# Optimization experiments

Hardware: AMD Instinct MI355X
Metric: run time of the kernel (lower is better)

Reference implementation:

```python
import jax, jax.numpy as jnp
import numpy as np

B, C, R, E, H = 32, 64, 63, 256, 4
D = E // H  # head dim = 64


def setup_inputs() -> dict:
    key = jax.random.key(0)
    ks = jax.random.split(key, 8)
    s = 0.02
    return {
        "x": jax.random.normal(ks[0], (B, C, R, E), jnp.float32),
        "real_cols": jax.random.randint(ks[1], (B,), 0, C),
        "cls_token": jax.random.normal(ks[2], (E,), jnp.float32),
        "w_in": (jax.random.normal(ks[3], (3 * E, E), jnp.float32) * s),
        "b_in": jnp.zeros((3 * E,), jnp.float32),
        "w_out": (jax.random.normal(ks[4], (E, E), jnp.float32) * s),
        "b_out": jnp.zeros((E,), jnp.float32),
        "ln_g": jnp.ones((E,), jnp.float32),
        "ln_b": jnp.zeros((E,), jnp.float32),
        "w1": (jax.random.normal(ks[5], (E, E), jnp.float32) * s),
        "b1": jnp.zeros((E,), jnp.float32),
        "w2": (jax.random.normal(ks[6], (E, E), jnp.float32) * s),
        "b2": jnp.zeros((E,), jnp.float32),
    }


def reference(x, real_cols, cls_token, w_in, b_in, w_out, b_out, ln_g, ln_b, w1, b1, w2, b2):
    # x: (B, C, R, E); one fused batched MHA+LN+FFN over all (B, C) columns.
    Bq, Cq, Rq, Eq = x.shape
    S = Rq + 1
    cls = jnp.broadcast_to(cls_token, (Bq, Cq, 1, Eq))
    seq = jnp.concatenate([cls, x], axis=2)  # (B,C,S,E)

    # torch MultiheadAttention in-projection: x @ W^T + b, packed q|k|v
    qkv = seq @ w_in.T + b_in  # (B,C,S,3E)
    q, k, v = jnp.split(qkv, 3, axis=-1)
    q = q.reshape(Bq, Cq, S, H, D)
    k = k.reshape(Bq, Cq, S, H, D)
    v = v.reshape(Bq, Cq, S, H, D)

    scale = 1.0 / jnp.sqrt(jnp.asarray(D, x.dtype))
    scores = jnp.einsum('bcqhd,bckhd->bchqk', q, k) * scale  # (B,C,H,S,S)
    attn = jax.nn.softmax(scores, axis=-1)
    ctx = jnp.einsum('bchqk,bckhd->bcqhd', attn, v).reshape(Bq, Cq, S, Eq)
    attn_out = ctx @ w_out.T + b_out  # (B,C,S,E)

    # LayerNorm (biased variance, eps=1e-5 as in torch)
    mu = attn_out.mean(axis=-1, keepdims=True)
    var = ((attn_out - mu) ** 2).mean(axis=-1, keepdims=True)
    ln = (attn_out - mu) / jnp.sqrt(var + 1e-5) * ln_g + ln_b

    ffn = jax.nn.relu(ln @ w1.T + b1) @ w2.T + b2
    out = ln + ffn  # (B,C,S,E)

    rep = out[:, :, 0, :]  # rep_mode == 'cls'

    # columns >= real_cols[b] are zero-padded, matching the original loop
    mask = jnp.arange(Cq)[None, :] < real_cols[:, None]
    return jnp.where(mask[..., None], rep, jnp.zeros((), x.dtype))
```

## Files before the change

### kernel.cpp

```cpp
#include <hip/hip_runtime.h>
#include <hip/hip_bf16.h>
#include <cstdint>

typedef unsigned short u16;
typedef uint32_t u32;

#define Bq 32
#define Cq 64
#define Rq 63
#define NB 4
#define SEQ_ST 264

typedef __attribute__((ext_vector_type(8))) short bf16x8;
typedef __attribute__((ext_vector_type(4))) float f32x4;

__device__ __forceinline__ float bflo(u32 u){ return __uint_as_float(u << 16); }
__device__ __forceinline__ float bfhi(u32 u){ return __uint_as_float(u & 0xffff0000u); }
__device__ __forceinline__ float bf1(u16 u){ return __uint_as_float(((u32)u) << 16); }
__device__ __forceinline__ u16 tobf(float f){ __hip_bfloat16 h = __float2bfloat16(f); return *(u16*)&h; }

__device__ __forceinline__ bool dtype_is_bf16(const void* ln_g){
    return *(const u32*)ln_g == 0x3F803F80u;
}
__device__ __forceinline__ float ldin(const void* p, int i, bool bf){
    return bf ? bf1(((const u16*)p)[i]) : ((const float*)p)[i];
}


__global__ __launch_bounds__(256) void prep_kernel(
    const void* __restrict__ cls, const void* __restrict__ w_in,
    const void* __restrict__ b_in, const void* __restrict__ w_out,
    const void* __restrict__ w1, const void* __restrict__ w2,
    const void* __restrict__ ln_g_flag,
    float* __restrict__ uf, float* __restrict__ sbf,
    u16* __restrict__ wvT, u16* __restrict__ woT,
    u16* __restrict__ w1T, u16* __restrict__ w2T)
{
    const bool bf = dtype_is_bf16(ln_g_flag);
    const int tid = threadIdx.x;
    const int blk = blockIdx.x;
    __shared__ float q0[256];
    __shared__ __align__(16) float clsf[256];

    if (blk < 256) {
        const int e = blk, j = tid;
        const int dsti = (((e >> 4) * 512) + ((j >> 5) * 64) + (((j >> 3) & 3) * 16) + (e & 15)) * 8 + (j & 7);
        wvT[dsti] = tobf(ldin(w_in, (512 + e) * 256 + j, bf));
        woT[dsti] = tobf(ldin(w_out, e * 256 + j, bf));
        w1T[dsti] = tobf(ldin(w1,    e * 256 + j, bf));
        w2T[dsti] = tobf(ldin(w2,    e * 256 + j, bf));
        return;
    }

    const int h = blk - 256;
    clsf[tid] = ldin(cls, tid, bf);
    __syncthreads();

    {
        float acc = ldin(b_in, tid, bf);
        if (bf) {
            const u16* wr = (const u16*)w_in + tid * 256;
            #pragma unroll 8
            for (int j8 = 0; j8 < 32; ++j8) {
                uint4 w = *(const uint4*)(wr + j8 * 8);
                const float* c = &clsf[j8 * 8];
                acc += bflo(w.x) * c[0] + bfhi(w.x) * c[1]
                     + bflo(w.y) * c[2] + bfhi(w.y) * c[3]
                     + bflo(w.z) * c[4] + bfhi(w.z) * c[5]
                     + bflo(w.w) * c[6] + bfhi(w.w) * c[7];
            }
        } else {
            const float4* wr = (const float4*)((const float*)w_in + tid * 256);
            #pragma unroll 8
            for (int j4 = 0; j4 < 64; ++j4) {
                float4 w = wr[j4];
                float4 c = *(const float4*)&clsf[j4 * 4];
                acc += w.x * c.x + w.y * c.y + w.z * c.z + w.w * c.w;
            }
        }
        q0[tid] = acc;
    }
    __syncthreads();

    {
        float ua = 0.f;
        #pragma unroll 8
        for (int d = 0; d < 64; ++d)
            ua += q0[h * 64 + d] * ldin(w_in, (256 + h * 64 + d) * 256 + tid, bf);
        uf[h * 256 + tid] = ua * 0.125f;
    }
    if (tid < 64) {
        float p = q0[h * 64 + tid] * ldin(b_in, 256 + h * 64 + tid, bf);
        #pragma unroll
        for (int off = 32; off; off >>= 1) p += __shfl_xor(p, off);
        if (tid == 0) sbf[h] = p * 0.125f;
    }
}

__device__ __forceinline__ void mfma_layer4(const u16* __restrict__ wbase,
                                            const u16* __restrict__ Abase,
                                            int lane, int w,
                                            f32x4 acc[4])
{
    bf16x8 af[8];
    const u16* ap = Abase + (lane & 15) * SEQ_ST + (lane >> 4) * 8;
    #pragma unroll
    for (int ks = 0; ks < 8; ++ks)
        af[ks] = *(const bf16x8*)(ap + ks * 32);
    const u16* wp0 = wbase + (((w * 4) * 512 + lane) << 3);
    #pragma unroll
    for (int ks = 0; ks < 8; ++ks) {
        #pragma unroll
        for (int nt = 0; nt < 4; ++nt) {
            bf16x8 bfr = *(const bf16x8*)(wp0 + ((nt * 512 + ks * 64) << 3));
            acc[nt] = __builtin_amdgcn_mfma_f32_16x16x32_bf16(af[ks], bfr, acc[nt], 0, 0, 0);
        }
    }
}

__global__ __launch_bounds__(256) void fused_kernel(
    const void* __restrict__ x, const int* __restrict__ real_cols,
    const void* __restrict__ cls,
    const void* __restrict__ b_in, const void* __restrict__ b_out,
    const void* __restrict__ ln_g, const void* __restrict__ ln_b,
    const void* __restrict__ b1p, const void* __restrict__ b2p,
    const float* __restrict__ uf, const float* __restrict__ sbf,
    const u16* __restrict__ wvT, const u16* __restrict__ woT,
    const u16* __restrict__ w1T, const u16* __restrict__ w2T,
    void* __restrict__ out)
{
    const bool bf = dtype_is_bf16(ln_g);
    const int tid = threadIdx.x;
    const int b = blockIdx.x >> 4;
    const int g = blockIdx.x & 15;
    const int c0 = g * NB;
    const int rc = real_cols[b];
    const int e = tid;

    if (c0 >= rc) {
        #pragma unroll
        for (int i = 0; i < NB; ++i) {
            size_t oi = (((size_t)b << 6) + c0 + i) * 256 + e;
            if (bf) ((u16*)out)[oi] = 0; else ((float*)out)[oi] = 0.f;
        }
        return;
    }

    __shared__ __align__(16) char smem[53840];
    u16*   seq    = (u16*)smem;
    u16*   ctxB   = (u16*)smem;
    float* aoF    = (float*)(smem + 8448);
    u16*   lnB    = (u16*)(smem + 12544);
    u16*   h1B    = (u16*)(smem + 20992);
    float* lds_u  = (float*)(smem + 33792);
    float* lds_a  = (float*)(smem + 37888);
    float* lds_sb = (float*)(smem + 38912);
    u16*   sB     = (u16*)(smem + 38928);
    float* redA   = (float*)(smem + 53712);
    float* redB   = (float*)(smem + 53776);

    #pragma unroll
    for (int q = 0; q < 4; ++q) lds_u[q * 256 + tid] = uf[q * 256 + tid];
    if (tid < 4) lds_sb[tid] = sbf[tid];

    if (bf) {
        if (tid < 32) {
            uint4 val = *(const uint4*)((const u16*)cls + tid * 8);
            *(uint4*)&seq[tid * 8] = val;
        }
    } else {
        if (tid < 64) {
            float4 v = *(const float4*)((const float*)cls + tid * 4);
            u32 lo = ((u32)tobf(v.y) << 16) | tobf(v.x);
            u32 hi = ((u32)tobf(v.w) << 16) | tobf(v.z);
            *(uint2*)&seq[tid * 4] = make_uint2(lo, hi);
        }
    }

    const int w = tid >> 6, lane = tid & 63;

    uint4 stg[8];
    float4 stgf[16];
    auto load_col = [&](int c) {
        int bc2 = (b << 6) + c;
        if (bf) {
            const u16* xr = (const u16*)x + (size_t)bc2 * (Rq * 256);
            #pragma unroll
            for (int k = 0; k < 8; ++k) {
                int idx = k * 256 + tid;
                if (idx < 2016) stg[k] = *(const uint4*)(xr + idx * 8);
            }
        } else {
            const float* xr = (const float*)x + (size_t)bc2 * (Rq * 256);
            #pragma unroll
            for (int k = 0; k < 16; ++k) {
                int idx = k * 256 + tid;
                if (idx < 4032) stgf[k] = *(const float4*)(xr + idx * 4);
            }
        }
    };
    auto write_col = [&]() {
        if (bf) {
            #pragma unroll
            for (int k = 0; k < 8; ++k) {
                int idx = k * 256 + tid;
                if (idx < 2016) {
                    int tt = (idx >> 5) + 1, col = (idx & 31) * 8;
                    *(uint4*)&seq[tt * SEQ_ST + col] = stg[k];
                }
            }
        } else {
            #pragma unroll
            for (int k = 0; k < 16; ++k) {
                int idx = k * 256 + tid;
                if (idx < 4032) {
                    float4 v = stgf[k];
                    int tt = (idx >> 6) + 1, col = (idx & 63) * 4;
                    u32 lo = ((u32)tobf(v.y) << 16) | tobf(v.x);
                    u32 hi = ((u32)tobf(v.w) << 16) | tobf(v.z);
                    *(uint2*)&seq[tt * SEQ_ST + col] = make_uint2(lo, hi);
                }
            }
        }
    };

    load_col(c0);

    for (int i = 0; i < NB; ++i) {
        const int c = c0 + i;
        const bool act = (c < rc);

        if (act) write_col();
        __syncthreads();

        if (i + 1 < NB && c0 + i + 1 < rc) load_col(c0 + i + 1);

        if (act) {
            float sc = lds_sb[w];
            {
                const u16* srow = &seq[lane * SEQ_ST];
                const float* uh = &lds_u[w * 256];
                #pragma unroll 4
                for (int j = 0; j < 256; j += 8) {
                    uint4 pv = *(const uint4*)(srow + j);
                    float4 u0 = *(const float4*)(uh + j);
                    float4 u1 = *(const float4*)(uh + j + 4);
                    sc += bflo(pv.x) * u0.x + bfhi(pv.x) * u0.y
                        + bflo(pv.y) * u0.z + bfhi(pv.y) * u0.w
                        + bflo(pv.z) * u1.x + bfhi(pv.z) * u1.y
                        + bflo(pv.w) * u1.z + bfhi(pv.w) * u1.w;
                }
            }
            float m = sc;
            #pragma unroll
            for (int off = 32; off; off >>= 1) m = fmaxf(m, __shfl_xor(m, off));
            float ev = __expf(sc - m);
            float sum = ev;
            #pragma unroll
            for (int off = 32; off; off >>= 1) sum += __shfl_xor(sum, off);
            lds_a[lane * 4 + w] = ev / sum;
        }
        __syncthreads();

        if (act) {
            float s0 = 0.f, s1 = 0.f, s2 = 0.f, s3 = 0.f;
            #pragma unroll 4
            for (int tt = 0; tt < 64; ++tt) {
                float v = bf1(seq[tt * SEQ_ST + tid]);
                float4 at = *(const float4*)&lds_a[tt * 4];
                s0 += at.x * v; s1 += at.y * v; s2 += at.z * v; s3 += at.w * v;
            }
            sB[(0  + i) * SEQ_ST + tid] = tobf(s0);
            sB[(4  + i) * SEQ_ST + tid] = tobf(s1);
            sB[(8  + i) * SEQ_ST + tid] = tobf(s2);
            sB[(12 + i) * SEQ_ST + tid] = tobf(s3);
        } else {
            sB[(0  + i) * SEQ_ST + tid] = 0;
            sB[(4  + i) * SEQ_ST + tid] = 0;
            sB[(8  + i) * SEQ_ST + tid] = 0;
            sB[(12 + i) * SEQ_ST + tid] = 0;
        }
        __syncthreads();
    }

    f32x4 acc[4];

    #pragma unroll
    for (int nt = 0; nt < 4; ++nt) {
        float bv = ldin(b_in, 512 + w * 64 + nt * 16 + (lane & 15), bf);
        acc[nt] = (f32x4){bv, bv, bv, bv};
    }
    mfma_layer4(wvT, sB + w * 4 * SEQ_ST, lane, w, acc);
    if (lane < 16) {
        #pragma unroll
        for (int nt = 0; nt < 4; ++nt) {
            int n = w * 64 + nt * 16 + lane;
            #pragma unroll
            for (int r = 0; r < 4; ++r) ctxB[r * SEQ_ST + n] = tobf(acc[nt][r]);
        }
    }
    __syncthreads();

    #pragma unroll
    for (int nt = 0; nt < 4; ++nt) {
        float bv = ldin(b_out, w * 64 + nt * 16 + (lane & 15), bf);
        acc[nt] = (f32x4){bv, bv, bv, bv};
    }
    mfma_layer4(woT, ctxB, lane, w, acc);
    if (lane < 16) {
        #pragma unroll
        for (int nt = 0; nt < 4; ++nt) {
            int n = w * 64 + nt * 16 + lane;
            #pragma unroll
            for (int r = 0; r < 4; ++r) aoF[r * 256 + n] = acc[nt][r];
        }
    }
    __syncthreads();

    float ao[NB];
    #pragma unroll
    for (int i = 0; i < NB; ++i) ao[i] = aoF[i * 256 + e];

    float mu[NB];
    {
        float r[NB];
        #pragma unroll
        for (int i = 0; i < NB; ++i) r[i] = ao[i];
        #pragma unroll
        for (int off = 32; off; off >>= 1) {
            #pragma unroll
            for (int i = 0; i < NB; ++i) r[i] += __shfl_xor(r[i], off);
        }
        if (lane == 0) {
            #pragma unroll
            for (int i = 0; i < NB; ++i) redA[w * NB + i] = r[i];
        }
    }
    __syncthreads();
    #pragma unroll
    for (int i = 0; i < NB; ++i)
        mu[i] = (redA[i] + redA[NB + i] + redA[2 * NB + i] + redA[3 * NB + i]) * (1.f / 256.f);

    float lnv[NB];
    {
        float r[NB];
        #pragma unroll
        for (int i = 0; i < NB; ++i) { float d = ao[i] - mu[i]; r[i] = d * d; }
        #pragma unroll
        for (int off = 32; off; off >>= 1) {
            #pragma unroll
            for (int i = 0; i < NB; ++i) r[i] += __shfl_xor(r[i], off);
        }
        if (lane == 0) {
            #pragma unroll
            for (int i = 0; i < NB; ++i) redB[w * NB + i] = r[i];
        }
    }
    __syncthreads();
    {
        float gg = ldin(ln_g, e, bf), bb = ldin(ln_b, e, bf);
        #pragma unroll
        for (int i = 0; i < NB; ++i) {
            float var = (redB[i] + redB[NB + i] + redB[2 * NB + i] + redB[3 * NB + i]) * (1.f / 256.f);
            lnv[i] = (ao[i] - mu[i]) * rsqrtf(var + 1e-5f) * gg + bb;
            lnB[i * SEQ_ST + e] = tobf(lnv[i]);
        }
    }
    __syncthreads();

    #pragma unroll
    for (int nt = 0; nt < 4; ++nt) {
        float bv = ldin(b1p, w * 64 + nt * 16 + (lane & 15), bf);
        acc[nt] = (f32x4){bv, bv, bv, bv};
    }
    mfma_layer4(w1T, lnB, lane, w, acc);
    if (lane < 16) {
        #pragma unroll
        for (int nt = 0; nt < 4; ++nt) {
            int n = w * 64 + nt * 16 + lane;
            #pragma unroll
            for (int r = 0; r < 4; ++r) h1B[r * SEQ_ST + n] = tobf(fmaxf(acc[nt][r], 0.f));
        }
    }
    __syncthreads();

    #pragma unroll
    for (int nt = 0; nt < 4; ++nt) {
        float bv = ldin(b2p, w * 64 + nt * 16 + (lane & 15), bf);
        acc[nt] = (f32x4){bv, bv, bv, bv};
    }
    mfma_layer4(w2T, h1B, lane, w, acc);
    float* oF = aoF;
    if (lane < 16) {
        #pragma unroll
        for (int nt = 0; nt < 4; ++nt) {
            int n = w * 64 + nt * 16 + lane;
            #pragma unroll
            for (int r = 0; r < 4; ++r) oF[r * 256 + n] = acc[nt][r];
        }
    }
    __syncthreads();

    #pragma unroll
    for (int i = 0; i < NB; ++i) {
        int c = c0 + i;
        float val = (c < rc) ? (oF[i * 256 + e] + lnv[i]) : 0.f;
        size_t oi = (((size_t)b << 6) + c) * 256 + e;
        if (bf) ((u16*)out)[oi] = tobf(val); else ((float*)out)[oi] = val;
    }
}

extern "C" void kernel_launch(void* const* d_in, const int* in_sizes, int n_in,
                              void* d_out, int out_size, void* d_ws, size_t ws_size,
                              hipStream_t stream) {
    const void* x     = d_in[0];
    const int* rcols  = (const int*)d_in[1];
    const void* cls   = d_in[2];
    const void* w_in  = d_in[3];
    const void* b_in  = d_in[4];
    const void* w_out = d_in[5];
    const void* b_out = d_in[6];
    const void* ln_g  = d_in[7];
    const void* ln_b  = d_in[8];
    const void* w1    = d_in[9];
    const void* b1    = d_in[10];
    const void* w2    = d_in[11];
    const void* b2    = d_in[12];

    char* ws = (char*)d_ws;
    float* uf  = (float*)(ws);
    float* sbf = (float*)(ws + 4096);
    u16* wvT = (u16*)(ws + 4608);
    u16* woT = (u16*)(ws + 4608 + 131072);
    u16* w1T = (u16*)(ws + 4608 + 2 * 131072);
    u16* w2T = (u16*)(ws + 4608 + 3 * 131072);

    prep_kernel<<<260, 256, 0, stream>>>(cls, w_in, b_in, w_out, w1, w2, ln_g,
                                         uf, sbf, wvT, woT, w1T, w2T);
    fused_kernel<<<Bq * (Cq / NB), 256, 0, stream>>>(x, rcols, cls,
                                                     b_in, b_out, ln_g, ln_b,
                                                     b1, b2, uf, sbf,
                                                     wvT, woT, w1T, w2T, d_out);
}
```

Baseline: 233.7 us.

## Compute CLS attention scores with MFMA and cross-wave split softmax

The CLS-query attention scores were a scalar per-lane dot product over 256 elements against an fp32 u vector. They are now one 16x16x32 bf16 MFMA tile per wave against a bf16 u matrix, pre-laid out and zero-padded in the prep kernel. Because each wave now covers 16 tokens for all heads, the softmax becomes a two-stage reduction with partial max and sum exchanged through LDS, which adds a barrier. The constant score bias term sbf is dropped, which is harmless since it cancels in softmax. u is quantised to bf16, which reduces precision.

```diff
diff --git a/kernel.cpp b/kernel.cpp
--- a/kernel.cpp
+++ b/kernel.cpp
@@ -32,7 +32,7 @@
     const void* __restrict__ b_in, const void* __restrict__ w_out,
     const void* __restrict__ w1, const void* __restrict__ w2,
     const void* __restrict__ ln_g_flag,
-    float* __restrict__ uf, float* __restrict__ sbf,
+    u16* __restrict__ uB,
     u16* __restrict__ wvT, u16* __restrict__ woT,
     u16* __restrict__ w1T, u16* __restrict__ w2T)
 {
@@ -84,16 +84,16 @@
 
     {
         float ua = 0.f;
+        const int j = tid;
         #pragma unroll 8
         for (int d = 0; d < 64; ++d)
-            ua += q0[h * 64 + d] * ldin(w_in, (256 + h * 64 + d) * 256 + tid, bf);
-        uf[h * 256 + tid] = ua * 0.125f;
-    }
-    if (tid < 64) {
-        float p = q0[h * 64 + tid] * ldin(b_in, 256 + h * 64 + tid, bf);
-        #pragma unroll
-        for (int off = 32; off; off >>= 1) p += __shfl_xor(p, off);
-        if (tid == 0) sbf[h] = p * 0.125f;
+            ua += q0[h * 64 + d] * ldin(w_in, (256 + h * 64 + d) * 256 + j, bf);
+        const int base = ((j >> 5) * 64) + (((j >> 3) & 3) * 16);
+        const int ii = j & 7;
+        uB[(base + h)      * 8 + ii] = tobf(ua * 0.125f);
+        uB[(base + h + 4)  * 8 + ii] = 0;
+        uB[(base + h + 8)  * 8 + ii] = 0;
+        uB[(base + h + 12) * 8 + ii] = 0;
     }
 }
 
@@ -124,7 +124,7 @@
     const void* __restrict__ b_in, const void* __restrict__ b_out,
     const void* __restrict__ ln_g, const void* __restrict__ ln_b,
     const void* __restrict__ b1p, const void* __restrict__ b2p,
-    const float* __restrict__ uf, const float* __restrict__ sbf,
+    const u16* __restrict__ uBg,
     const u16* __restrict__ wvT, const u16* __restrict__ woT,
     const u16* __restrict__ w1T, const u16* __restrict__ w2T,
     void* __restrict__ out)
@@ -146,22 +146,22 @@
         return;
     }
 
-    __shared__ __align__(16) char smem[53840];
+    __shared__ __align__(16) char smem[58048];
     u16*   seq    = (u16*)smem;
     u16*   ctxB   = (u16*)smem;
     float* aoF    = (float*)(smem + 8448);
     u16*   lnB    = (u16*)(smem + 12544);
     u16*   h1B    = (u16*)(smem + 20992);
-    float* lds_u  = (float*)(smem + 33792);
-    float* lds_a  = (float*)(smem + 37888);
-    float* lds_sb = (float*)(smem + 38912);
-    u16*   sB     = (u16*)(smem + 38928);
-    float* redA   = (float*)(smem + 53712);
-    float* redB   = (float*)(smem + 53776);
-
-    #pragma unroll
-    for (int q = 0; q < 4; ++q) lds_u[q * 256 + tid] = uf[q * 256 + tid];
-    if (tid < 4) lds_sb[tid] = sbf[tid];
+    u16*   uB     = (u16*)(smem + 33792);
+    float* lds_a  = (float*)(smem + 41984);
+    u16*   sB     = (u16*)(smem + 43008);
+    float* redA   = (float*)(smem + 57792);
+    float* redB   = (float*)(smem + 57856);
+    float* redPm  = (float*)(smem + 57920);
+    float* redPs  = (float*)(smem + 57984);
+
+    ((uint4*)uB)[tid]       = ((const uint4*)uBg)[tid];
+    ((uint4*)uB)[tid + 256] = ((const uint4*)uBg)[tid + 256];
 
     if (bf) {
         if (tid < 32) {
@@ -235,30 +235,45 @@
 
         if (i + 1 < NB && c0 + i + 1 < rc) load_col(c0 + i + 1);
 
+        float mw, ev0, ev1, ev2, ev3;
         if (act) {
-            float sc = lds_sb[w];
-            {
-                const u16* srow = &seq[lane * SEQ_ST];
-                const float* uh = &lds_u[w * 256];
-                #pragma unroll 4
-                for (int j = 0; j < 256; j += 8) {
-                    uint4 pv = *(const uint4*)(srow + j);
-                    float4 u0 = *(const float4*)(uh + j);
-                    float4 u1 = *(const float4*)(uh + j + 4);
-                    sc += bflo(pv.x) * u0.x + bfhi(pv.x) * u0.y
-                        + bflo(pv.y) * u0.z + bfhi(pv.y) * u0.w
-                        + bflo(pv.z) * u1.x + bfhi(pv.z) * u1.y
-                        + bflo(pv.w) * u1.z + bfhi(pv.w) * u1.w;
-                }
-            }
-            float m = sc;
-            #pragma unroll
-            for (int off = 32; off; off >>= 1) m = fmaxf(m, __shfl_xor(m, off));
-            float ev = __expf(sc - m);
-            float sum = ev;
-            #pragma unroll
-            for (int off = 32; off; off >>= 1) sum += __shfl_xor(sum, off);
-            lds_a[lane * 4 + w] = ev / sum;
+            const u16* ap = &seq[(w * 16 + (lane & 15)) * SEQ_ST + (lane >> 4) * 8];
+            f32x4 cacc = (f32x4){0.f, 0.f, 0.f, 0.f};
+            #pragma unroll
+            for (int ks = 0; ks < 8; ++ks) {
+                bf16x8 a  = *(const bf16x8*)(ap + ks * 32);
+                bf16x8 bb = *(const bf16x8*)(uB + ((ks * 64 + lane) << 3));
+                cacc = __builtin_amdgcn_mfma_f32_16x16x32_bf16(a, bb, cacc, 0, 0, 0);
+            }
+            mw = fmaxf(fmaxf(cacc[0], cacc[1]), fmaxf(cacc[2], cacc[3]));
+            mw = fmaxf(mw, __shfl_xor(mw, 16));
+            mw = fmaxf(mw, __shfl_xor(mw, 32));
+            ev0 = __expf(cacc[0] - mw); ev1 = __expf(cacc[1] - mw);
+            ev2 = __expf(cacc[2] - mw); ev3 = __expf(cacc[3] - mw);
+            float sw = ev0 + ev1 + ev2 + ev3;
+            sw += __shfl_xor(sw, 16);
+            sw += __shfl_xor(sw, 32);
+            if (lane < 4) { redPm[w * 4 + lane] = mw; redPs[w * 4 + lane] = sw; }
+        }
+        __syncthreads();
+
+        if (act) {
+            const int h2 = lane & 15;
+            if (h2 < 4) {
+                float m0 = redPm[h2],     m1 = redPm[4 + h2];
+                float m2 = redPm[8 + h2], m3 = redPm[12 + h2];
+                float M = fmaxf(fmaxf(m0, m1), fmaxf(m2, m3));
+                float S = redPs[h2]      * __expf(m0 - M)
+                        + redPs[4 + h2]  * __expf(m1 - M)
+                        + redPs[8 + h2]  * __expf(m2 - M)
+                        + redPs[12 + h2] * __expf(m3 - M);
+                float corr = __expf(mw - M) / S;
+                int t0 = (w * 16 + (lane >> 4) * 4) * 4 + h2;
+                lds_a[t0]      = ev0 * corr;
+                lds_a[t0 + 4]  = ev1 * corr;
+                lds_a[t0 + 8]  = ev2 * corr;
+                lds_a[t0 + 12] = ev3 * corr;
+            }
         }
         __syncthreads();
 
@@ -428,17 +443,16 @@
     const void* b2    = d_in[12];
 
     char* ws = (char*)d_ws;
-    float* uf  = (float*)(ws);
-    float* sbf = (float*)(ws + 4096);
-    u16* wvT = (u16*)(ws + 4608);
-    u16* woT = (u16*)(ws + 4608 + 131072);
-    u16* w1T = (u16*)(ws + 4608 + 2 * 131072);
-    u16* w2T = (u16*)(ws + 4608 + 3 * 131072);
+    u16* uB  = (u16*)(ws);
+    u16* wvT = (u16*)(ws + 8192);
+    u16* woT = (u16*)(ws + 8192 + 131072);
+    u16* w1T = (u16*)(ws + 8192 + 2 * 131072);
+    u16* w2T = (u16*)(ws + 8192 + 3 * 131072);
 
     prep_kernel<<<260, 256, 0, stream>>>(cls, w_in, b_in, w_out, w1, w2, ln_g,
-                                         uf, sbf, wvT, woT, w1T, w2T);
+                                         uB, wvT, woT, w1T, w2T);
     fused_kernel<<<Bq * (Cq / NB), 256, 0, stream>>>(x, rcols, cls,
                                                      b_in, b_out, ln_g, ln_b,
-                                                     b1, b2, uf, sbf,
+                                                     b1, b2, uB,
                                                      wvT, woT, w1T, w2T, d_out);
 }
```

Result: slower. 240.0 us (+2.7%).
